# Optimization experiments

Measured on AMD Instinct MI355X. Metric: run time of the kernel, lower is better.

Reference implementation:

```python
import jax, jax.numpy as jnp
import numpy as np

B, S, D, H = 8, 384, 768, 12
MAX_POS = 512
P = 2 * MAX_POS - 1  # 1023


def setup_inputs() -> dict:
    key = jax.random.key(0)
    ks = jax.random.split(key, 14)
    w = 0.02
    return {
        "x": jax.random.normal(ks[0], (B, S, D), jnp.float32),
        "rel_pos_emb": jax.random.normal(ks[1], (P, D), jnp.float32),
        "Wq": jax.random.normal(ks[2], (D, D), jnp.float32) * w,
        "bq": jax.random.normal(ks[3], (D,), jnp.float32) * w,
        "Wk": jax.random.normal(ks[4], (D, D), jnp.float32) * w,
        "bk": jax.random.normal(ks[5], (D,), jnp.float32) * w,
        "Wv": jax.random.normal(ks[6], (D, D), jnp.float32) * w,
        "bv": jax.random.normal(ks[7], (D,), jnp.float32) * w,
        "q_bias": jax.random.normal(ks[8], (D,), jnp.float32) * w,
        "v_bias": jax.random.normal(ks[9], (D,), jnp.float32) * w,
        "Wpk": jax.random.normal(ks[10], (D, D), jnp.float32) * w,
        "Wpq": jax.random.normal(ks[11], (D, D), jnp.float32) * w,
        "Wo": jax.random.normal(ks[12], (D, D), jnp.float32) * w,
        "bo": jax.random.normal(ks[13], (D,), jnp.float32) * w,
    }


def reference(x, rel_pos_emb, Wq, bq, Wk, bk, Wv, bv, q_bias, v_bias, Wpk, Wpq, Wo, bo):
    b, s, d = x.shape
    dh = d // H
    scale = dh ** -0.5
    # relative position index: rel[i, j] = j - i + MAX_POS - 1
    rel = (jnp.arange(s)[None, :] - jnp.arange(s)[:, None]) + MAX_POS - 1
    emb = rel_pos_emb[rel]                      # [S, S, D]
    q = (x @ Wq + bq + q_bias).reshape(b, s, H, dh)
    k = (x @ Wk + bk).reshape(b, s, H, dh)
    v = (x @ Wv + bv + v_bias).reshape(b, s, H, dh)
    Kp = (emb @ Wpk).reshape(s, s, H, dh)       # pos keys   [i, j, h, d]
    Qp = (emb @ Wpq).reshape(s, s, H, dh)       # pos queries[i, j, h, d]
    c2c = jnp.einsum('bihd,bjhd->bhij', q, k)
    c2p = jnp.einsum('bihd,ijhd->bhij', q, Kp)
    p2c = jnp.einsum('ijhd,bjhd->bhij', Qp, k)
    scores = (c2c + c2p + p2c) * scale          # [B, H, S, S]
    w = jax.nn.softmax(scores, axis=-1)
    out = jnp.einsum('bhij,bjhd->bihd', w, v).reshape(b, s, d)
    return out @ Wo + bo
```

## Files before the change

kernel.cpp:

```cpp
#include <hip/hip_runtime.h>
#include <hip/hip_bf16.h>
#include <math.h>

#define BATCH 8
#define SEQ 384
#define DIM 768
#define NH 12
#define DH 64
#define NPOS 767
#define POS_OFF 128
#define NTOK (BATCH * SEQ)
#define QKN 1536
#define QKVN 2304
#define PN 1536

typedef __attribute__((ext_vector_type(8))) short short8;
typedef __attribute__((ext_vector_type(4))) float floatx4;
typedef unsigned int u32;

__device__ __forceinline__ ushort f2bf(float f) {
    __hip_bfloat16 h = __float2bfloat16(f);
    return *reinterpret_cast<ushort*>(&h);
}
__device__ __forceinline__ float bf2f(ushort u) {
    u32 x = ((u32)u) << 16;
    float f; __builtin_memcpy(&f, &x, 4); return f;
}

__device__ __forceinline__ void gld16(const ushort* g, ushort* l) {
    __builtin_amdgcn_global_load_lds(
        (const __attribute__((address_space(1))) u32*)g,
        (__attribute__((address_space(3))) u32*)l, 16, 0, 0);
}

#define MFMA __builtin_amdgcn_mfma_f32_16x16x32_bf16

__global__ __launch_bounds__(256) void prep(
    const float* W0, const float* W1, const float* W2,
    const float* W3, const float* W4, const float* W5,
    const float* x, const float* rpe,
    ushort* __restrict__ wsT, ushort* __restrict__ xb, ushort* __restrict__ rpeb)
{
    const int tid = threadIdx.x;
    if (blockIdx.z < 6) {
        __shared__ float t[64][65];
        const float* srcs[6] = {W0, W1, W2, W3, W4, W5};
        const float* in = srcs[blockIdx.z];
        ushort* out = wsT + (size_t)blockIdx.z * DIM * DIM;
        const int r0 = blockIdx.y * 64, c0 = blockIdx.x * 64;
        for (int p = 0; p < 16; ++p) {
            int e = tid + p * 256, i = e >> 6, j = e & 63;
            t[i][j] = in[(size_t)(r0 + i) * DIM + c0 + j];
        }
        __syncthreads();
        for (int p = 0; p < 16; ++p) {
            int e = tid + p * 256, i = e >> 6, j = e & 63;
            out[(size_t)(c0 + i) * DIM + r0 + j] = f2bf(t[j][i]);
        }
    } else {
        const int n4x = NTOK * DIM / 4;
        const int n4p = NPOS * DIM / 4;
        const int fb = blockIdx.y * 12 + blockIdx.x;
        for (int idx = fb * 256 + tid; idx < n4x + n4p; idx += 144 * 256) {
            const float* src; ushort* dst; int j;
            if (idx < n4x) { src = x; dst = xb; j = idx; }
            else { src = rpe + (size_t)POS_OFF * DIM; dst = rpeb; j = idx - n4x; }
            float4 f = ((const float4*)src)[j];
            ushort o[4] = {f2bf(f.x), f2bf(f.y), f2bf(f.z), f2bf(f.w)};
            *(uint2*)&dst[(size_t)j * 4] = *(uint2*)o;
        }
    }
}

__global__ __launch_bounds__(256) void proj_all(
    const ushort* __restrict__ xb, const ushort* __restrict__ rpeb,
    const ushort* __restrict__ wsT,
    const float* __restrict__ bq, const float* __restrict__ qbias,
    const float* __restrict__ bk, const float* __restrict__ bv,
    const float* __restrict__ vbias,
    ushort* __restrict__ qk, ushort* __restrict__ vT, ushort* __restrict__ posKQ)
{
    __shared__ ushort As[128 * 64];
    __shared__ ushort Bs[128 * 64];
    const int tid = threadIdx.x;
    const int lane = tid & 63, w = tid >> 6;
    const int id = blockIdx.x;
    const bool qkvP = id < 432;
    const ushort* A; const ushort* Bt; int m0, n0, M;
    if (qkvP) {
        m0 = (id % 24) * 128; n0 = (id / 24) * 128;
        A = xb; Bt = wsT; M = NTOK;
    } else {
        int p = id - 432;
        m0 = (p % 6) * 128; n0 = (p / 6) * 128;
        A = rpeb; Bt = wsT + (size_t)3 * DIM * DIM; M = NPOS;
    }
    const int lr = lane >> 3;
    const int lc = (lane & 7) ^ (lr & 7);
    const ushort* ga[4]; const ushort* gb[4];
#pragma unroll
    for (int p = 0; p < 4; ++p) {
        int row = (w * 4 + p) * 8 + lr;
        int arow = m0 + row; if (arow > M - 1) arow = M - 1;
        ga[p] = A + (size_t)arow * DIM + lc * 8;
        gb[p] = Bt + (size_t)(n0 + row) * DIM + lc * 8;
    }
    floatx4 acc[4][4] = {};
    const int qr = (w >> 1) * 64, qc = (w & 1) * 64;
    const int lm = lane & 15, lk = lane >> 4;
    for (int k0 = 0; k0 < DIM; k0 += 64) {
#pragma unroll
        for (int p = 0; p < 4; ++p) {
            gld16(ga[p], As + (w * 4 + p) * 512);
            gld16(gb[p], Bs + (w * 4 + p) * 512);
            ga[p] += 64; gb[p] += 64;
        }
        __syncthreads();
#pragma unroll
        for (int kk = 0; kk < 2; ++kk) {
            int ch = (kk * 4 + lk) ^ (lm & 7);
            short8 af[4], bf[4];
#pragma unroll
            for (int t = 0; t < 4; ++t) {
                af[t] = *(const short8*)&As[(qr + t * 16 + lm) * 64 + ch * 8];
                bf[t] = *(const short8*)&Bs[(qc + t * 16 + lm) * 64 + ch * 8];
            }
#pragma unroll
            for (int i = 0; i < 4; ++i)
#pragma unroll
                for (int j = 0; j < 4; ++j)
                    acc[i][j] = MFMA(af[i], bf[j], acc[i][j], 0, 0, 0);
        }
        __syncthreads();
    }
    if (qkvP) {
#pragma unroll
        for (int i = 0; i < 4; ++i) {
            int mbase = m0 + qr + i * 16 + (lane >> 4) * 4;
            int bb = mbase / SEQ;
            int s0 = mbase - bb * SEQ;
#pragma unroll
            for (int j = 0; j < 4; ++j) {
                int n = n0 + qc + j * 16 + lm;
                float bs;
                if (n < 768) bs = bq[n] + qbias[n];
                else if (n < QKN) bs = bk[n - 768];
                else bs = bv[n - QKN] + vbias[n - QKN];
                if (n < QKN) {
#pragma unroll
                    for (int r = 0; r < 4; ++r)
                        qk[(size_t)(mbase + r) * QKN + n] = f2bf(acc[i][j][r] + bs);
                } else {
                    int c = n - QKN, h = c >> 6, d = c & 63;
                    ushort tmp[4];
#pragma unroll
                    for (int r = 0; r < 4; ++r) tmp[r] = f2bf(acc[i][j][r] + bs);
                    *(uint2*)&vT[(((size_t)bb * NH + h) * DH + d) * SEQ + s0] = *(uint2*)tmp;
                }
            }
        }
    } else {
#pragma unroll
        for (int i = 0; i < 4; ++i) {
            int mbase = m0 + qr + i * 16 + (lane >> 4) * 4;
#pragma unroll
            for (int j = 0; j < 4; ++j) {
                int n = n0 + qc + j * 16 + lm;
#pragma unroll
                for (int r = 0; r < 4; ++r) {
                    int row = mbase + r;
                    if (row < NPOS)
                        posKQ[(size_t)row * PN + n] = f2bf(acc[i][j][r]);
                }
            }
        }
    }
}

__global__ __launch_bounds__(256) void gemm128x64(
    const ushort* __restrict__ A, const ushort* __restrict__ Bt,
    const float* __restrict__ bias, float* __restrict__ outF,
    int M, int N, int K)
{
    __shared__ ushort As[128 * 64];
    __shared__ ushort Bs[64 * 64];
    const int tid = threadIdx.x;
    const int lane = tid & 63, w = tid >> 6;
    const int n0 = blockIdx.x * 64, m0 = blockIdx.y * 128;
    const int lr = lane >> 3;
    const int lc = (lane & 7) ^ (lr & 7);
    const ushort* ga[4]; const ushort* gb[2];
#pragma unroll
    for (int p = 0; p < 4; ++p) {
        int arow = m0 + (w * 4 + p) * 8 + lr; if (arow > M - 1) arow = M - 1;
        ga[p] = A + (size_t)arow * K + lc * 8;
    }
#pragma unroll
    for (int p = 0; p < 2; ++p)
        gb[p] = Bt + (size_t)(n0 + (w * 2 + p) * 8 + lr) * K + lc * 8;
    floatx4 acc[4][2] = {};
    const int qr = (w >> 1) * 64, qc = (w & 1) * 32;
    const int lm = lane & 15, lk = lane >> 4;
    for (int k0 = 0; k0 < K; k0 += 64) {
#pragma unroll
        for (int p = 0; p < 4; ++p) { gld16(ga[p], As + (w * 4 + p) * 512); ga[p] += 64; }
#pragma unroll
        for (int p = 0; p < 2; ++p) { gld16(gb[p], Bs + (w * 2 + p) * 512); gb[p] += 64; }
        __syncthreads();
#pragma unroll
        for (int kk = 0; kk < 2; ++kk) {
            int ch = (kk * 4 + lk) ^ (lm & 7);
            short8 af[4], bf[2];
#pragma unroll
            for (int t = 0; t < 4; ++t)
                af[t] = *(const short8*)&As[(qr + t * 16 + lm) * 64 + ch * 8];
#pragma unroll
            for (int t = 0; t < 2; ++t)
                bf[t] = *(const short8*)&Bs[(qc + t * 16 + lm) * 64 + ch * 8];
#pragma unroll
            for (int i = 0; i < 4; ++i)
#pragma unroll
                for (int j = 0; j < 2; ++j)
                    acc[i][j] = MFMA(af[i], bf[j], acc[i][j], 0, 0, 0);
        }
        __syncthreads();
    }
#pragma unroll
    for (int i = 0; i < 4; ++i) {
        int mbase = m0 + qr + i * 16 + (lane >> 4) * 4;
#pragma unroll
        for (int j = 0; j < 2; ++j) {
            int n = n0 + qc + j * 16 + lm;
            float bs = bias[n];
#pragma unroll
            for (int r = 0; r < 4; ++r) {
                int row = mbase + r;
                if (row < M) outF[(size_t)row * N + n] = acc[i][j][r] + bs;
            }
        }
    }
}

__global__ __launch_bounds__(512, 2) void attn_fused8(
    const ushort* __restrict__ qk, const ushort* __restrict__ vT,
    const ushort* __restrict__ posKQ, ushort* __restrict__ aob)
{
    __shared__ ushort kt[64 * 64];
    __shared__ ushort kps[128 * 64];
    __shared__ ushort qps[128 * 64];
    __shared__ ushort ccpt[2][64 * 72];
    __shared__ ushort dqs[64 * 72];
    __shared__ ushort dks[64 * 72];
    __shared__ float rowsum[64];

    const int tid = threadIdx.x;
    const int lane = tid & 63, w = tid >> 6;
    const int i0 = blockIdx.x * 64;
    const int h = blockIdx.y, b = blockIdx.z;
    const int lm = lane & 15, lq = lane >> 4;
    const int lr = lane >> 3, l8 = lane & 7;
    const int lc = l8 ^ (lr & 7);
    const int exr = tid >> 3, exseg = tid & 7;

    if (tid < 64) rowsum[tid] = 0.f;

    short8 qf[2];
    {
        const ushort* qr = qk + (size_t)(b * SEQ + i0 + (w >> 1) * 16 + lm) * QKN + h * DH;
        qf[0] = *(const short8*)(qr + lq * 8);
        qf[1] = *(const short8*)(qr + 32 + lq * 8);
    }
    const ushort* kb = qk + 768 + h * DH;
    floatx4 occ[2] = {};

    {
        int t0 = 0 - i0 + 320;
        gld16(kb + (size_t)(b * SEQ + 8 * w + lr) * QKN + lc * 8, kt + w * 512);
        gld16(posKQ + (size_t)(t0 + 16 * w + lr) * PN + h * DH + lc * 8, kps + w * 1024);
        gld16(posKQ + (size_t)(t0 + 16 * w + 8 + lr) * PN + h * DH + lc * 8, kps + w * 1024 + 512);
        gld16(posKQ + (size_t)(t0 + 16 * w + lr) * PN + 768 + h * DH + lc * 8, qps + w * 1024);
        gld16(posKQ + (size_t)(t0 + 16 * w + 8 + lr) * PN + 768 + h * DH + lc * 8, qps + w * 1024 + 512);
    }

    for (int jt = 0; jt < 6; ++jt) {
        const int j0 = jt * 64;
        ushort* cc = ccpt[jt & 1];
        __syncthreads();

        {
            int tr = w >> 1, tcb = (w & 1) * 2;
            floatx4 a[2] = {};
#pragma unroll
            for (int kk = 0; kk < 2; ++kk) {
                int ch = (kk * 4 + lq) ^ (lm & 7);
                short8 b0 = *(const short8*)&kt[(tcb * 16 + lm) * 64 + ch * 8];
                short8 b1 = *(const short8*)&kt[((tcb + 1) * 16 + lm) * 64 + ch * 8];
                a[0] = MFMA(qf[kk], b0, a[0], 0, 0, 0);
                a[1] = MFMA(qf[kk], b1, a[1], 0, 0, 0);
            }
#pragma unroll
            for (int s = 0; s < 2; ++s) {
                int j = (tcb + s) * 16 + lm;
#pragma unroll
                for (int r = 0; r < 4; ++r)
                    cc[(tr * 16 + lq * 4 + r) * 72 + j] = f2bf(a[s][r]);
            }
        }
        {
            int tr = w >> 1, tcb = (w & 1) * 4;
            floatx4 d[4] = {};
#pragma unroll
            for (int kk = 0; kk < 2; ++kk) {
                int ch = (kk * 4 + lq) ^ (lm & 7);
#pragma unroll
                for (int s = 0; s < 4; ++s) {
                    short8 bf = *(const short8*)&kps[((tcb + s) * 16 + lm) * 64 + ch * 8];
                    d[s] = MFMA(qf[kk], bf, d[s], 0, 0, 0);
                }
            }
#pragma unroll
            for (int s = 0; s < 4; ++s) {
                int t = (tcb + s) * 16 + lm;
#pragma unroll
                for (int r = 0; r < 4; ++r) {
                    int i = tr * 16 + lq * 4 + r;
                    int j = t + i - 63;
                    if ((unsigned)j < 64u) dqs[i * 72 + j] = f2bf(d[s][r]);
                }
            }
        }
        {
            floatx4 e[4] = {};
#pragma unroll
            for (int kk = 0; kk < 2; ++kk) {
                int ch = (kk * 4 + lq) ^ (lm & 7);
                short8 af = *(const short8*)&qps[(w * 16 + lm) * 64 + ch * 8];
#pragma unroll
                for (int s = 0; s < 4; ++s) {
                    short8 bf = *(const short8*)&kt[(s * 16 + lm) * 64 + ch * 8];
                    e[s] = MFMA(af, bf, e[s], 0, 0, 0);
                }
            }
#pragma unroll
            for (int s = 0; s < 4; ++s) {
                int j = s * 16 + lm;
#pragma unroll
                for (int r = 0; r < 4; ++r) {
                    int t = w * 16 + lq * 4 + r;
                    int i = j - t + 63;
                    if ((unsigned)i < 64u) dks[i * 72 + j] = f2bf(e[s][r]);
                }
            }
        }
        __syncthreads();

        if (jt < 5) {
            int j0n = j0 + 64;
            int t0n = j0n - i0 + 320;
            gld16(kb + (size_t)(b * SEQ + j0n + 8 * w + lr) * QKN + lc * 8, kt + w * 512);
            gld16(posKQ + (size_t)(t0n + 16 * w + lr) * PN + h * DH + lc * 8, kps + w * 1024);
            gld16(posKQ + (size_t)(t0n + 16 * w + 8 + lr) * PN + h * DH + lc * 8, kps + w * 1024 + 512);
            gld16(posKQ + (size_t)(t0n + 16 * w + lr) * PN + 768 + h * DH + lc * 8, qps + w * 1024);
            gld16(posKQ + (size_t)(t0n + 16 * w + 8 + lr) * PN + 768 + h * DH + lc * 8, qps + w * 1024 + 512);
        }

        {
            int off = exr * 72 + exseg * 8;
            uint4 c4 = *(const uint4*)&cc[off];
            uint4 q4 = *(const uint4*)&dqs[off];
            uint4 k4 = *(const uint4*)&dks[off];
            const ushort* cu = (const ushort*)&c4;
            const ushort* qu = (const ushort*)&q4;
            const ushort* ku = (const ushort*)&k4;
            float psum = 0.f;
            ushort pv[8];
#pragma unroll
            for (int c = 0; c < 8; ++c) {
                float sv = (bf2f(cu[c]) + bf2f(qu[c]) + bf2f(ku[c])) * 0.125f;
                float pe = __expf(sv);
                psum += pe;
                pv[c] = f2bf(pe);
            }
            psum += __shfl_xor(psum, 1);
            psum += __shfl_xor(psum, 2);
            psum += __shfl_xor(psum, 4);
            if (exseg == 0) rowsum[exr] += psum;
            *(uint4*)&cc[off] = *(uint4*)pv;
        }
        __syncthreads();

        {
            int tr = w >> 1, dtb = (w & 1) * 2;
#pragma unroll
            for (int t2 = 0; t2 < 2; ++t2) {
                int dt = dtb + t2;
                const ushort* vr = vT + ((size_t)(b * NH + h) * DH + dt * 16 + lm) * SEQ + j0;
                short8 vf0 = *(const short8*)(vr + lq * 8);
                short8 vf1 = *(const short8*)(vr + 32 + lq * 8);
                short8 af0 = *(const short8*)&cc[(tr * 16 + lm) * 72 + lq * 8];
                short8 af1 = *(const short8*)&cc[(tr * 16 + lm) * 72 + 32 + lq * 8];
                occ[t2] = MFMA(af0, vf0, occ[t2], 0, 0, 0);
                occ[t2] = MFMA(af1, vf1, occ[t2], 0, 0, 0);
            }
        }
    }

    {
        int tr = w >> 1, dtb = (w & 1) * 2;
#pragma unroll
        for (int t2 = 0; t2 < 2; ++t2) {
#pragma unroll
            for (int r = 0; r < 4; ++r) {
                int row = tr * 16 + lq * 4 + r;
                float ov = occ[t2][r] / rowsum[row];
                aob[(size_t)(b * SEQ + i0 + row) * DIM + h * DH + (dtb + t2) * 16 + lm] = f2bf(ov);
            }
        }
    }
}

extern "C" void kernel_launch(void* const* d_in, const int* in_sizes, int n_in,
                              void* d_out, int out_size, void* d_ws, size_t ws_size,
                              hipStream_t stream) {
    const float* x   = (const float*)d_in[0];
    const float* rpe = (const float*)d_in[1];
    const float* Wq  = (const float*)d_in[2];
    const float* bq  = (const float*)d_in[3];
    const float* Wk  = (const float*)d_in[4];
    const float* bk  = (const float*)d_in[5];
    const float* Wv  = (const float*)d_in[6];
    const float* bv  = (const float*)d_in[7];
    const float* qbias = (const float*)d_in[8];
    const float* vbias = (const float*)d_in[9];
    const float* Wpk = (const float*)d_in[10];
    const float* Wpq = (const float*)d_in[11];
    const float* Wo  = (const float*)d_in[12];
    const float* bo  = (const float*)d_in[13];
    float* out = (float*)d_out;

    char* ws = (char*)d_ws;
    ushort* xb    = (ushort*)ws; ws += (size_t)NTOK * DIM * 2;
    ushort* qkbuf = (ushort*)ws; ws += (size_t)NTOK * QKN * 2;
    ushort* vT    = (ushort*)ws; ws += (size_t)NTOK * DIM * 2;
    ushort* aob   = (ushort*)ws; ws += (size_t)NTOK * DIM * 2;
    ushort* rpeb  = (ushort*)ws; ws += (size_t)NPOS * DIM * 2;
    ushort* posKQ = (ushort*)ws; ws += (size_t)NPOS * PN * 2;
    ushort* wsT   = (ushort*)ws; ws += (size_t)6 * DIM * DIM * 2;

    prep<<<dim3(12, 12, 7), dim3(256), 0, stream>>>(
        Wq, Wk, Wv, Wpk, Wpq, Wo, x, rpe, wsT, xb, rpeb);
    proj_all<<<dim3(504), dim3(256), 0, stream>>>(
        xb, rpeb, wsT, bq, qbias, bk, bv, vbias, qkbuf, vT, posKQ);
    attn_fused8<<<dim3(SEQ / 64, NH, BATCH), dim3(512), 0, stream>>>(qkbuf, vT, posKQ, aob);
    gemm128x64<<<dim3(DIM / 64, NTOK / 128), dim3(256), 0, stream>>>(
        aob, wsT + (size_t)5 * DIM * DIM, bo, out, NTOK, DIM, DIM);
}
```

Measured before the change: 182.1 us.

## Load positional K/Q fragments directly into registers instead of LDS staging

Each wave now loads its positional key and query MFMA operands straight from global memory into registers at the start of every tile, so the kps/qps shared-memory buffers go away. The launch bounds rise from 2 to 6 blocks per CU to use the LDS that is freed. The aim is less LDS traffic and footprint and more resident blocks. In exchange, the global loads are issued right before the barrier with no prefetch across iterations, which may expose latency, and the higher occupancy target limits registers per thread.

```diff
diff --git a/kernel.cpp b/kernel.cpp
--- a/kernel.cpp
+++ b/kernel.cpp
@@ -241,13 +241,11 @@
     }
 }
 
-__global__ __launch_bounds__(512, 2) void attn_fused8(
+__global__ __launch_bounds__(512, 6) void attn_fused9(
     const ushort* __restrict__ qk, const ushort* __restrict__ vT,
     const ushort* __restrict__ posKQ, ushort* __restrict__ aob)
 {
     __shared__ ushort kt[64 * 64];
-    __shared__ ushort kps[128 * 64];
-    __shared__ ushort qps[128 * 64];
     __shared__ ushort ccpt[2][64 * 72];
     __shared__ ushort dqs[64 * 72];
     __shared__ ushort dks[64 * 72];
@@ -273,51 +271,59 @@
     const ushort* kb = qk + 768 + h * DH;
     floatx4 occ[2] = {};
 
-    {
-        int t0 = 0 - i0 + 320;
-        gld16(kb + (size_t)(b * SEQ + 8 * w + lr) * QKN + lc * 8, kt + w * 512);
-        gld16(posKQ + (size_t)(t0 + 16 * w + lr) * PN + h * DH + lc * 8, kps + w * 1024);
-        gld16(posKQ + (size_t)(t0 + 16 * w + 8 + lr) * PN + h * DH + lc * 8, kps + w * 1024 + 512);
-        gld16(posKQ + (size_t)(t0 + 16 * w + lr) * PN + 768 + h * DH + lc * 8, qps + w * 1024);
-        gld16(posKQ + (size_t)(t0 + 16 * w + 8 + lr) * PN + 768 + h * DH + lc * 8, qps + w * 1024 + 512);
-    }
+    const int t0i = 0 - i0 + 320;
+    const int tcb = (w & 1) * 4;
+    const ushort* kp_p[4];
+#pragma unroll
+    for (int s = 0; s < 4; ++s)
+        kp_p[s] = posKQ + (size_t)(t0i + (tcb + s) * 16 + lm) * PN + h * DH + lq * 8;
+    const ushort* qp_p = posKQ + (size_t)(t0i + w * 16 + lm) * PN + 768 + h * DH + lq * 8;
+
+    gld16(kb + (size_t)(b * SEQ + 8 * w + lr) * QKN + lc * 8, kt + w * 512);
 
     for (int jt = 0; jt < 6; ++jt) {
         const int j0 = jt * 64;
         ushort* cc = ccpt[jt & 1];
+
+        short8 kpf[2][4];
+        short8 qpf[2];
+#pragma unroll
+        for (int kk = 0; kk < 2; ++kk) {
+#pragma unroll
+            for (int s = 0; s < 4; ++s)
+                kpf[kk][s] = *(const short8*)(kp_p[s] + kk * 32);
+            qpf[kk] = *(const short8*)(qp_p + kk * 32);
+        }
+
         __syncthreads();
 
         {
-            int tr = w >> 1, tcb = (w & 1) * 2;
+            int tr = w >> 1, tjb = (w & 1) * 2;
             floatx4 a[2] = {};
 #pragma unroll
             for (int kk = 0; kk < 2; ++kk) {
                 int ch = (kk * 4 + lq) ^ (lm & 7);
-                short8 b0 = *(const short8*)&kt[(tcb * 16 + lm) * 64 + ch * 8];
-                short8 b1 = *(const short8*)&kt[((tcb + 1) * 16 + lm) * 64 + ch * 8];
+                short8 b0 = *(const short8*)&kt[(tjb * 16 + lm) * 64 + ch * 8];
+                short8 b1 = *(const short8*)&kt[((tjb + 1) * 16 + lm) * 64 + ch * 8];
                 a[0] = MFMA(qf[kk], b0, a[0], 0, 0, 0);
                 a[1] = MFMA(qf[kk], b1, a[1], 0, 0, 0);
             }
 #pragma unroll
             for (int s = 0; s < 2; ++s) {
-                int j = (tcb + s) * 16 + lm;
+                int j = (tjb + s) * 16 + lm;
 #pragma unroll
                 for (int r = 0; r < 4; ++r)
                     cc[(tr * 16 + lq * 4 + r) * 72 + j] = f2bf(a[s][r]);
             }
         }
         {
-            int tr = w >> 1, tcb = (w & 1) * 4;
+            int tr = w >> 1;
             floatx4 d[4] = {};
 #pragma unroll
-            for (int kk = 0; kk < 2; ++kk) {
-                int ch = (kk * 4 + lq) ^ (lm & 7);
-#pragma unroll
-                for (int s = 0; s < 4; ++s) {
-                    short8 bf = *(const short8*)&kps[((tcb + s) * 16 + lm) * 64 + ch * 8];
-                    d[s] = MFMA(qf[kk], bf, d[s], 0, 0, 0);
-                }
-            }
+            for (int kk = 0; kk < 2; ++kk)
+#pragma unroll
+                for (int s = 0; s < 4; ++s)
+                    d[s] = MFMA(qf[kk], kpf[kk][s], d[s], 0, 0, 0);
 #pragma unroll
             for (int s = 0; s < 4; ++s) {
                 int t = (tcb + s) * 16 + lm;
@@ -334,11 +340,10 @@
 #pragma unroll
             for (int kk = 0; kk < 2; ++kk) {
                 int ch = (kk * 4 + lq) ^ (lm & 7);
-                short8 af = *(const short8*)&qps[(w * 16 + lm) * 64 + ch * 8];
 #pragma unroll
                 for (int s = 0; s < 4; ++s) {
                     short8 bf = *(const short8*)&kt[(s * 16 + lm) * 64 + ch * 8];
-                    e[s] = MFMA(af, bf, e[s], 0, 0, 0);
+                    e[s] = MFMA(qpf[kk], bf, e[s], 0, 0, 0);
                 }
             }
 #pragma unroll
@@ -355,14 +360,11 @@
         __syncthreads();
 
         if (jt < 5) {
-            int j0n = j0 + 64;
-            int t0n = j0n - i0 + 320;
-            gld16(kb + (size_t)(b * SEQ + j0n + 8 * w + lr) * QKN + lc * 8, kt + w * 512);
-            gld16(posKQ + (size_t)(t0n + 16 * w + lr) * PN + h * DH + lc * 8, kps + w * 1024);
-            gld16(posKQ + (size_t)(t0n + 16 * w + 8 + lr) * PN + h * DH + lc * 8, kps + w * 1024 + 512);
-            gld16(posKQ + (size_t)(t0n + 16 * w + lr) * PN + 768 + h * DH + lc * 8, qps + w * 1024);
-            gld16(posKQ + (size_t)(t0n + 16 * w + 8 + lr) * PN + 768 + h * DH + lc * 8, qps + w * 1024 + 512);
-        }
+            gld16(kb + (size_t)(b * SEQ + j0 + 64 + 8 * w + lr) * QKN + lc * 8, kt + w * 512);
+        }
+#pragma unroll
+        for (int s = 0; s < 4; ++s) kp_p[s] += 64 * PN;
+        qp_p += 64 * PN;
 
         {
             int off = exr * 72 + exseg * 8;
@@ -451,7 +453,7 @@
         Wq, Wk, Wv, Wpk, Wpq, Wo, x, rpe, wsT, xb, rpeb);
     proj_all<<<dim3(504), dim3(256), 0, stream>>>(
         xb, rpeb, wsT, bq, qbias, bk, bv, vbias, qkbuf, vT, posKQ);
-    attn_fused8<<<dim3(SEQ / 64, NH, BATCH), dim3(512), 0, stream>>>(qkbuf, vT, posKQ, aob);
+    attn_fused9<<<dim3(SEQ / 64, NH, BATCH), dim3(512), 0, stream>>>(qkbuf, vT, posKQ, aob);
     gemm128x64<<<dim3(DIM / 64, NTOK / 128), dim3(256), 0, stream>>>(
         aob, wsT + (size_t)5 * DIM * DIM, bo, out, NTOK, DIM, DIM);
 }
```

Measured after the change: 304.4 us. 1.67x slower.
